# Kernel tuning notes

Hardware: AMD Instinct MI355X
Metric: run time of the kernel (lower is better)

The kernel has to match this reference:

```python
import jax, jax.numpy as jnp
import numpy as np

B, N, D, L = 64, 2047, 512, 4
T = D + 1        # token_dim = d + 1
H = 512          # hidden_dim
LN_EPS = 1e-5
ATTN_EPS = 1e-6


def setup_inputs() -> dict:
    key = jax.random.key(0)
    ks = jax.random.split(key, 10)
    s = 0.01  # matches xavier_uniform_ gain=0.01 small-init magnitude
    return dict(
        xs=jax.random.normal(ks[0], (B, N, D), jnp.float32),
        ys=jax.random.normal(ks[1], (B, N), jnp.float32),
        query_x=jax.random.normal(ks[2], (B, 1, D), jnp.float32),
        Wq=jax.random.normal(ks[3], (L, H, T), jnp.float32) * s,
        Wk=jax.random.normal(ks[4], (L, H, T), jnp.float32) * s,
        Wv=jax.random.normal(ks[5], (L, T, T), jnp.float32) * s,
        Wo=jax.random.normal(ks[6], (L, T, T), jnp.float32) * s,
        ln1_w=jnp.ones((L, T), jnp.float32),
        ln1_b=jnp.zeros((L, T), jnp.float32),
        ln2_w=jnp.ones((L, T), jnp.float32),
        ln2_b=jnp.zeros((L, T), jnp.float32),
        scale=jnp.ones((L,), jnp.float32),
        pred_w=jax.random.normal(ks[7], (1, T), jnp.float32) * 0.02,
    )


def _ln(x, w, b):
    m = jnp.mean(x, axis=-1, keepdims=True)
    v = jnp.var(x, axis=-1, keepdims=True)
    return (x - m) * jax.lax.rsqrt(v + LN_EPS) * w + b


def _l2norm(x):
    n = jnp.sqrt(jnp.sum(x * x, axis=-1, keepdims=True))
    return x / jnp.maximum(n, 1e-12)


def _forward(xs, ys, query_x, Wq, Wk, Wv, Wo, ln1_w, ln1_b, ln2_w, ln2_b, scale, pred_w):
    b = xs.shape[0]
    train_tokens = jnp.concatenate([xs, ys[..., None]], axis=-1)          # [B,N,T]
    query_token = jnp.concatenate([query_x, jnp.zeros((b, 1, 1), xs.dtype)], axis=-1)
    tokens = jnp.concatenate([train_tokens, query_token], axis=1)          # [B,N+1,T]

    def step(tok, p):
        wq, wk, wv, wo, w1, b1, w2, b2, sc = p
        x = _ln(tok, w1, b1)
        Q = jnp.einsum('bnt,ht->bnh', x, wq)
        K = jnp.einsum('bnt,ht->bnh', x, wk)
        V = jnp.einsum('bnt,ut->bnu', x, wv)
        Q = _l2norm(Q)
        K = _l2norm(K)
        s = jax.nn.softplus(sc)
        Qp = (jax.nn.elu(Q) + 1.0) * s
        Kp = jax.nn.elu(K) + 1.0
        KV = jnp.einsum('bnh,bnu->bhu', Kp, V)      # [B,H,T]
        Ksum = jnp.sum(Kp, axis=1)                  # [B,H]
        denom = jnp.einsum('bnh,bh->bn', Qp, Ksum)  # [B,N+1]
        attn = jnp.einsum('bnh,bhu->bnu', Qp, KV) / (denom[..., None] + ATTN_EPS)
        out = jnp.einsum('bnu,tu->bnt', attn, wo) * 0.1 + tok
        return _ln(out, w2, b2), None

    tokens, _ = jax.lax.scan(step, tokens, (Wq, Wk, Wv, Wo, ln1_w, ln1_b, ln2_w, ln2_b, scale))
    q_out = tokens[:, -1, :]                        # [B,T]
    return jnp.einsum('bt,ot->bo', q_out, pred_w)[..., 0]  # [B]


def reference(xs, ys, query_x, Wq, Wk, Wv, Wo, ln1_w, ln1_b, ln2_w, ln2_b, scale, pred_w):
    return _forward(xs, ys, query_x, Wq, Wk, Wv, Wo, ln1_w, ln1_b, ln2_w, ln2_b, scale, pred_w)
```

## Files before the change

kernel.cpp:

```cpp
#include <hip/hip_runtime.h>
#include <cstdint>
#include <cstddef>


typedef unsigned short u16;
typedef float f32x4 __attribute__((ext_vector_type(4)));
typedef unsigned short u16x8 __attribute__((ext_vector_type(8)));

#define P 576
#define NQK 1664
#define VTROWS 514
#define KVLD 640

__device__ __forceinline__ float bf2f(u16 s) {
    union { unsigned u; float f; } v; v.u = ((unsigned)s) << 16; return v.f;
}
__device__ __forceinline__ u16 f2bf(float f) {
    union { float f; unsigned u; } v; v.f = f;
    unsigned r = v.u + 0x7FFF + ((v.u >> 16) & 1);
    return (u16)(r >> 16);
}
__device__ __forceinline__ float wredsum(float v) {
#pragma unroll
    for (int o = 32; o > 0; o >>= 1) v += __shfl_xor(v, o, 64);
    return v;
}
__device__ __forceinline__ f32x4 mfma_16x16x32_bf16(u16x8 a, u16x8 b, f32x4 c) {
    asm volatile("v_mfma_f32_16x16x32_bf16 %0, %1, %2, %0"
                 : "+v"(c) : "v"(a), "v"(b));
    return c;
}
__device__ __forceinline__ void gload_lds16(const u16* g, u16* l) {
    __builtin_amdgcn_global_load_lds(
        (const __attribute__((address_space(1))) void*)g,
        (__attribute__((address_space(3))) void*)l, 16, 0, 0);
}

__global__ __launch_bounds__(256) void k_build_tokens(
    const float* __restrict__ xs, const float* __restrict__ ys,
    const float* __restrict__ qx, u16* __restrict__ tok,
    float* __restrict__ meanb, float* __restrict__ rstdb)
{
    long row = (long)blockIdx.x * 4 + (threadIdx.x >> 6);
    int lane = threadIdx.x & 63;
    int b = (int)(row >> 11), n = (int)(row & 2047);
    const float* src = (n < 2047) ? xs + ((long)(b * 2047 + n)) * 512
                                  : qx + (long)b * 512;
    float4 f0 = *(const float4*)(src + lane * 8);
    float4 f1 = *(const float4*)(src + lane * 8 + 4);
    float y = (n < 2047) ? ys[(long)b * 2047 + n] : 0.f;
    float v[8] = {f0.x, f0.y, f0.z, f0.w, f1.x, f1.y, f1.z, f1.w};
    float s = 0.f, sq = 0.f;
#pragma unroll
    for (int j = 0; j < 8; j++) { s += v[j]; sq += v[j] * v[j]; }
    if (lane == 0) { s += y; sq += y * y; }
    s = wredsum(s); sq = wredsum(sq);
    u16x8 o;
#pragma unroll
    for (int j = 0; j < 8; j++) o[j] = f2bf(v[j]);
    *(u16x8*)(tok + row * P + lane * 8) = o;
    if (lane < 8) {
        u16x8 z8 = {0,0,0,0,0,0,0,0};
        if (lane == 0) z8[0] = f2bf(y);
        *(u16x8*)(tok + row * P + 512 + lane * 8) = z8;
    }
    if (lane == 0) {
        float m = s * (1.f / 513.f);
        float var = sq * (1.f / 513.f) - m * m;
        meanb[row] = m;
        rstdb[row] = 1.f / sqrtf(var + 1e-5f);
    }
}

__global__ __launch_bounds__(256) void k_prep_wcat(
    const float* __restrict__ wq, const float* __restrict__ wk,
    const float* __restrict__ wv, const float* __restrict__ ln1w,
    u16* __restrict__ wcat)
{
    long idx = (long)blockIdx.x * 256 + threadIdx.x;
    if (idx >= 4L * NQK * P) return;
    int t = (int)(idx % P);
    long rem = idx / P;
    int r = (int)(rem % NQK);
    int l = (int)(rem / NQK);
    float v = 0.f;
    if (t < 513) {
        float wsc = ln1w[l * 513 + t];
        if (r < 512)       v = wq[((long)l * 512 + r) * 513 + t] * wsc;
        else if (r < 1024) v = wk[((long)l * 512 + (r - 512)) * 513 + t] * wsc;
        else if (r < 1537) v = wv[((long)l * 513 + (r - 1024)) * 513 + t] * wsc;
    }
    wcat[idx] = f2bf(v);
}

__global__ __launch_bounds__(256) void k_prep_wo(
    const float* __restrict__ wo, u16* __restrict__ wop)
{
    long idx = (long)blockIdx.x * 256 + threadIdx.x;
    if (idx >= 4L * P * P) return;
    int u = (int)(idx % P);
    long rem = idx / P;
    int t = (int)(rem % P);
    int l = (int)(rem / P);
    float v = (t < 513 && u < 513) ? wo[((long)l * 513 + t) * 513 + u] : 0.f;
    wop[idx] = f2bf(v);
}

__global__ __launch_bounds__(256) void k_prep_sums(
    const float* __restrict__ wq, const float* __restrict__ wk,
    const float* __restrict__ wv, const float* __restrict__ ln1w,
    const float* __restrict__ ln1b, float* __restrict__ s1, float* __restrict__ s2)
{
    int id = blockIdx.x * 4 + (threadIdx.x >> 6);
    int lane = threadIdx.x & 63;
    int l = id / NQK, r = id % NQK;
    float a1 = 0.f, a2 = 0.f;
    for (int t = lane; t < 513; t += 64) {
        float wc = 0.f;
        if (r < 512)       wc = wq[((long)l * 512 + r) * 513 + t];
        else if (r < 1024) wc = wk[((long)l * 512 + (r - 512)) * 513 + t];
        else if (r < 1537) wc = wv[((long)l * 513 + (r - 1024)) * 513 + t];
        a1 += ln1w[l * 513 + t] * wc;
        a2 += ln1b[l * 513 + t] * wc;
    }
    a1 = wredsum(a1); a2 = wredsum(a2);
    if (lane == 0) { s1[id] = a1; s2[id] = a2; }
}

__global__ __launch_bounds__(256) void k_ln2(
    const u16* __restrict__ z, u16* __restrict__ tok,
    const float* __restrict__ w, const float* __restrict__ bia,
    float* __restrict__ meanb, float* __restrict__ rstdb)
{
    long row = (long)blockIdx.x * 4 + (threadIdx.x >> 6);
    int lane = threadIdx.x & 63;
    const u16* zp = z + row * P;
    u16* tp = tok + row * P;
    u16x8 a0 = *(const u16x8*)(zp + lane * 8);
    u16x8 a1 = {0,0,0,0,0,0,0,0};
    if (lane < 8) a1 = *(const u16x8*)(zp + 512 + lane * 8);
    float v0[8], v1[8];
#pragma unroll
    for (int j = 0; j < 8; j++) v0[j] = bf2f(a0[j]);
#pragma unroll
    for (int j = 0; j < 8; j++) v1[j] = (lane < 8) ? bf2f(a1[j]) : 0.f;
    float s = 0.f, sq = 0.f;
#pragma unroll
    for (int j = 0; j < 8; j++) { s += v0[j]; sq += v0[j] * v0[j]; }
#pragma unroll
    for (int j = 0; j < 8; j++) { s += v1[j]; sq += v1[j] * v1[j]; }
    s = wredsum(s); sq = wredsum(sq);
    float mean = s * (1.f / 513.f);
    float var = sq * (1.f / 513.f) - mean * mean;
    float rstd = 1.f / sqrtf(var + 1e-5f);
    float so = 0.f, so2 = 0.f;
    u16x8 o0;
    float of0[8];
#pragma unroll
    for (int j = 0; j < 8; j++) {
        int t = lane * 8 + j;
        of0[j] = (v0[j] - mean) * rstd * w[t] + bia[t];
        so += of0[j]; so2 += of0[j] * of0[j];
        o0[j] = f2bf(of0[j]);
    }
    float of1[8];
#pragma unroll
    for (int j = 0; j < 8; j++) {
        int t = 512 + lane * 8 + j;
        float ov = 0.f;
        if (lane < 8 && t < 513) ov = (v1[j] - mean) * rstd * w[t] + bia[t];
        of1[j] = ov;
        so += ov; so2 += ov * ov;
    }
    so = wredsum(so); so2 = wredsum(so2);
    *(u16x8*)(tp + lane * 8) = o0;
    if (lane < 8) {
        u16x8 o1;
#pragma unroll
        for (int j = 0; j < 8; j++) o1[j] = f2bf(of1[j]);
        *(u16x8*)(tp + 512 + lane * 8) = o1;
    }
    if (lane == 0) {
        float m2 = so * (1.f / 513.f);
        float v2 = so2 * (1.f / 513.f) - m2 * m2;
        meanb[row] = m2;
        rstdb[row] = 1.f / sqrtf(v2 + 1e-5f);
    }
}

__global__ __launch_bounds__(256) void k_qknorm(
    u16* __restrict__ qkv, float* __restrict__ rkout,
    const float* __restrict__ scale, int l)
{
    long row = (long)blockIdx.x * 4 + (threadIdx.x >> 6);
    int lane = threadIdx.x & 63;
    float s = log1pf(expf(scale[l]));
    u16* rowp = qkv + row * NQK;
    u16x8 q8 = *(const u16x8*)(rowp + lane * 8);
    u16x8 k8 = *(const u16x8*)(rowp + 512 + lane * 8);
    float qf[8];
    float sqv = 0.f, skv = 0.f;
#pragma unroll
    for (int j = 0; j < 8; j++) { qf[j] = bf2f(q8[j]); sqv += qf[j] * qf[j]; }
#pragma unroll
    for (int j = 0; j < 8; j++) { float kf = bf2f(k8[j]); skv += kf * kf; }
    sqv = wredsum(sqv); skv = wredsum(skv);
    float rnq = 1.f / fmaxf(sqrtf(sqv), 1e-12f);
    float rnk = 1.f / fmaxf(sqrtf(skv), 1e-12f);
    u16x8 o;
#pragma unroll
    for (int j = 0; j < 8; j++) {
        float q = qf[j] * rnq;
        float qp = (q > 0.f) ? (q + 1.f) : expf(q);
        o[j] = f2bf(qp * s);
    }
    *(u16x8*)(rowp + lane * 8) = o;
    if (lane == 0) rkout[row] = rnk;
}

__global__ __launch_bounds__(256) void k_trans(
    const u16* __restrict__ qkv, const float* __restrict__ rk,
    u16* __restrict__ kpt)
{
    int ct = blockIdx.x;
    long r0 = (long)blockIdx.y * 64;
    int b = (int)(r0 >> 11);
    int nloc = (int)(r0 & 2047);
    int tid = threadIdx.x;
    int r = tid >> 2;
    int c0 = (tid & 3) * 16;
    __shared__ u16 T[64 * 80];
    const u16* src = qkv + (r0 + r) * NQK + 512 + ct * 64 + c0;
    u16x8 a = *(const u16x8*)src;
    u16x8 d = *(const u16x8*)(src + 8);
    float rkv = rk[r0 + r];
#pragma unroll
    for (int j = 0; j < 8; j++) {
        float kv = bf2f(a[j]) * rkv; kv = (kv > 0.f) ? kv + 1.f : expf(kv);
        T[(c0 + j) * 80 + r] = f2bf(kv);
    }
#pragma unroll
    for (int j = 0; j < 8; j++) {
        float kv = bf2f(d[j]) * rkv; kv = (kv > 0.f) ? kv + 1.f : expf(kv);
        T[(c0 + 8 + j) * 80 + r] = f2bf(kv);
    }
    __syncthreads();
    int orow = tid >> 2;
    int oc0 = (tid & 3) * 16;
    u16x8 w0 = *(const u16x8*)&T[orow * 80 + oc0];
    u16x8 w1 = *(const u16x8*)&T[orow * 80 + oc0 + 8];
    u16* dst = kpt + ((long)b * 512 + ct * 64 + orow) * 2048 + nloc + oc0;
    *(u16x8*)dst = w0;
    *(u16x8*)(dst + 8) = w1;
}

__global__ __launch_bounds__(512) void k_extract_ksum(
    const u16* __restrict__ kvh, float* __restrict__ ksum)
{
    int b = blockIdx.x, h = threadIdx.x;
    ksum[(long)b * 512 + h] = bf2f(kvh[((long)b * 512 + h) * KVLD + 513]);
}

__global__ __launch_bounds__(256) void k_denom(
    const u16* __restrict__ qkv, const float* __restrict__ ksum,
    float* __restrict__ denom)
{
    long row = (long)blockIdx.x * 4 + (threadIdx.x >> 6);
    int lane = threadIdx.x & 63;
    int b = (int)(row >> 11);
    u16x8 q = *(const u16x8*)(qkv + row * NQK + lane * 8);
    const float* ks = ksum + (long)b * 512 + lane * 8;
    float acc = 0.f;
#pragma unroll
    for (int j = 0; j < 8; j++) acc += bf2f(q[j]) * ks[j];
    acc = wredsum(acc);
    if (lane == 0) denom[row] = acc;
}

__global__ void k_predict(const u16* __restrict__ tok, const float* __restrict__ pw,
                          float* __restrict__ out)
{
    int b = blockIdx.x;
    int lane = threadIdx.x;
    const u16* rp = tok + ((long)b * 2048 + 2047) * P;
    float acc = 0.f;
    for (int t = lane; t < 513; t += 64) acc += bf2f(rp[t]) * pw[t];
    acc = wredsum(acc);
    if (lane == 0) out[b] = acc;
}

__global__ __launch_bounds__(256) void k_gemm_bt(
    const u16* __restrict__ A, const u16* __restrict__ Bt, u16* __restrict__ C,
    int M, int N, int K, int lda, int ldb, int ldc,
    long sA, long sB, long sC,
    const float* __restrict__ aux1, const float* __restrict__ aux2,
    const float* __restrict__ aux3, const float* __restrict__ aux4,
    long sAux, const u16* __restrict__ Res,
    float cscale, int mode, int r1, int padw,
    int ntm, int ntn, int nbz,
    u16* __restrict__ VT, int vtbase)
{
    int G = ntm * ntn * nbz;
    int id = blockIdx.x;
    int lin = (id & 7) * (G >> 3) + (id >> 3);
    int per = ntm * ntn;
    int bz = lin / per;
    int rem = lin - bz * per;
    int mt = rem / ntn;
    int nt = rem - mt * ntn;
    int m0 = mt * 128, n0 = nt * 128;

    A += (long)bz * sA; Bt += (long)bz * sB; C += (long)bz * sC;
    int tid = threadIdx.x, lane = tid & 63, w = tid >> 6;
    int wr = w >> 1, wc = w & 1;
    __shared__ u16 ldsbuf[2 * 128 * 64];
    u16* Als = ldsbuf;
    u16* Bls = ldsbuf + 128 * 64;
    __shared__ float auxR0[128], auxR1[128], auxA1[128];
    __shared__ float auxC0[128], auxC1[128], auxB1[128];

    if (tid < 128) {
        int gr = m0 + tid; if (gr >= M) gr = M - 1;
        float r0v = cscale, r1v = 0.f, a1v = 0.f;
        if (mode == 1) {
            const float* d1 = aux1 + (long)bz * sAux;
            r0v = cscale / (d1[gr] + 1e-6f);
        } else if (mode == 3) { r0v = aux1[gr]; r1v = aux2[gr]; }
        if (r1) a1v = bf2f(A[(long)gr * lda + K]);
        auxR0[tid] = r0v; auxR1[tid] = r1v; auxA1[tid] = a1v;
    } else {
        int t = tid - 128;
        int gc = n0 + t; if (gc >= N) gc = N - 1;
        float c0v = 0.f, c1v = 0.f, b1v = 0.f;
        if (mode == 3) { c0v = aux3[gc]; c1v = aux4[gc]; }
        if (r1) b1v = bf2f(Bt[(long)gc * ldb + K]);
        auxC0[t] = c0v; auxC1[t] = c1v; auxB1[t] = b1v;
    }

    f32x4 acc[4][4];
#pragma unroll
    for (int m = 0; m < 4; m++)
#pragma unroll
        for (int n = 0; n < 4; n++) { acc[m][n][0]=0.f; acc[m][n][1]=0.f; acc[m][n][2]=0.f; acc[m][n][3]=0.f; }

    int srow = lane >> 3;
    int scol = (lane & 7) * 8;
    int scolsw = scol ^ (srow << 3);
    int swz = (lane & 7) << 3;

    for (int k0 = 0; k0 < K; k0 += 64) {
#pragma unroll
        for (int i = 0; i < 4; i++) {
            int rt = (w * 4 + i) * 8 + srow;
            int gr = m0 + rt; gr = (gr < M) ? gr : (M - 1);
            gload_lds16(A + (long)gr * lda + k0 + scolsw, &Als[(w * 4 + i) * 512]);
        }
#pragma unroll
        for (int i = 0; i < 4; i++) {
            int rt = (w * 4 + i) * 8 + srow;
            int gc = n0 + rt; gc = (gc < N) ? gc : (N - 1);
            gload_lds16(Bt + (long)gc * ldb + k0 + scolsw, &Bls[(w * 4 + i) * 512]);
        }
        __syncthreads();
#pragma unroll
        for (int ks = 0; ks < 2; ks++) {
            u16x8 af[4], bfv[4];
#pragma unroll
            for (int m = 0; m < 4; m++) {
                int row = wr * 64 + m * 16 + (lane & 15);
                af[m] = *(const u16x8*)&Als[row * 64 + ((ks * 32 + (lane >> 4) * 8) ^ swz)];
            }
#pragma unroll
            for (int n = 0; n < 4; n++) {
                int col = wc * 64 + n * 16 + (lane & 15);
                bfv[n] = *(const u16x8*)&Bls[col * 64 + ((ks * 32 + (lane >> 4) * 8) ^ swz)];
            }
#pragma unroll
            for (int m = 0; m < 4; m++)
#pragma unroll
                for (int n = 0; n < 4; n++)
                    acc[m][n] = mfma_16x16x32_bf16(af[m], bfv[n], acc[m][n]);
        }
        __syncthreads();
    }

    bool isvt = (VT != nullptr) && (n0 >= vtbase);

    if (Res) {
        const u16* Rp = Res + (long)bz * sC;
#pragma unroll
        for (int i = 0; i < 8; i++) {
            int lrow = i * 16 + (tid >> 4);
            int lcol = (tid & 15) * 8;
            long gr = m0 + lrow; if (gr > (long)M - 1) gr = M - 1;
            long gcol = (long)n0 + lcol;
            long mx = (long)ldc - 8; if (gcol > mx) gcol = mx;
            *(u16x8*)&ldsbuf[lrow * 128 + lcol] = *(const u16x8*)&Rp[gr * ldc + gcol];
        }
        __syncthreads();
    }

    asm volatile("s_nop 7\n\ts_nop 7" ::: );

    if (!isvt) {
#pragma unroll
        for (int m = 0; m < 4; m++) {
            int lrbase = wr * 64 + m * 16 + ((lane >> 4) << 2);
#pragma unroll
            for (int n = 0; n < 4; n++) {
                int lc = wc * 64 + n * 16 + (lane & 15);
                float c0v = auxC0[lc], c1v = auxC1[lc], b1v = auxB1[lc];
#pragma unroll
                for (int r = 0; r < 4; r++) {
                    int lr = lrbase + r;
                    float wv = acc[m][n][r] + auxA1[lr] * b1v;
                    float v;
                    if (mode == 3) v = auxR1[lr] * (wv - auxR0[lr] * c0v) + c1v;
                    else {
                        v = wv * auxR0[lr];
                        if (Res) v += bf2f(ldsbuf[lr * 128 + lc]);
                    }
                    ldsbuf[lr * 128 + lc] = f2bf(v);
                }
            }
        }
        __syncthreads();

        int lcol = (tid & 15) * 8;
        int gc0 = n0 + lcol;
        bool colok = padw || (gc0 + 8 <= N);
#pragma unroll
        for (int i = 0; i < 8; i++) {
            int lrow = i * 16 + (tid >> 4);
            int gr = m0 + lrow;
            if (gr < M && colok) {
                *(u16x8*)&C[(long)gr * ldc + gc0] = *(const u16x8*)&ldsbuf[lrow * 128 + lcol];
            }
        }
    } else {
        int u0 = n0 - vtbase;
        int b = m0 >> 11;
        int nloc = m0 & 2047;
#pragma unroll
        for (int m = 0; m < 4; m++) {
            int lrbase = wr * 64 + m * 16 + ((lane >> 4) << 2);
#pragma unroll
            for (int n = 0; n < 4; n++) {
                int lc = wc * 64 + n * 16 + (lane & 15);
                float c0v = auxC0[lc], c1v = auxC1[lc];
#pragma unroll
                for (int r = 0; r < 4; r++) {
                    int lr = lrbase + r;
                    float wv = acc[m][n][r];
                    float v = (mode == 3) ? (auxR1[lr] * (wv - auxR0[lr] * c0v) + c1v)
                                          : (wv * auxR0[lr]);
                    ldsbuf[lc * 128 + (lr ^ ((lc & 7) << 3))] = f2bf(v);
                }
            }
        }
        __syncthreads();

        int nc = (tid & 15) * 8;
        const u16x8 ones = {0x3F80,0x3F80,0x3F80,0x3F80,0x3F80,0x3F80,0x3F80,0x3F80};
#pragma unroll
        for (int i = 0; i < 8; i++) {
            int ur = i * 16 + (tid >> 4);
            int u = u0 + ur;
            if (u < VTROWS) {
                u16x8 vv;
                if (u == 513) vv = ones;
                else vv = *(const u16x8*)&ldsbuf[ur * 128 + (nc ^ ((ur & 7) << 3))];
                *(u16x8*)&VT[((long)b * VTROWS + u) * 2048 + nloc + nc] = vv;
            }
        }
    }
}

extern "C" void kernel_launch(void* const* d_in, const int* in_sizes, int n_in,
                              void* d_out, int out_size, void* d_ws, size_t ws_size,
                              hipStream_t stream)
{
    const float* xs    = (const float*)d_in[0];
    const float* ys    = (const float*)d_in[1];
    const float* qx    = (const float*)d_in[2];
    const float* Wq    = (const float*)d_in[3];
    const float* Wk    = (const float*)d_in[4];
    const float* Wv    = (const float*)d_in[5];
    const float* Wo    = (const float*)d_in[6];
    const float* ln1w  = (const float*)d_in[7];
    const float* ln1b  = (const float*)d_in[8];
    const float* ln2w  = (const float*)d_in[9];
    const float* ln2b  = (const float*)d_in[10];
    const float* scale = (const float*)d_in[11];
    const float* predw = (const float*)d_in[12];
    float* out = (float*)d_out;

    char* ws = (char*)d_ws;
    u16*   tok   = (u16*)(ws + 0L);
    u16*   buf1  = (u16*)(ws + 150994944L);
    u16*   qkv   = (u16*)(ws + 301989888L);
    u16*   kpt   = (u16*)(ws + 738197504L);
    u16*   kvh   = (u16*)(ws + 872415232L);
    float* denom = (float*)(ws + 914358272L);
    float* meanb = (float*)(ws + 914882560L);
    float* rstdb = (float*)(ws + 915406848L);
    float* ksum  = (float*)(ws + 915931136L);
    u16*   wcat  = (u16*)(ws + 916062208L);
    u16*   wop   = (u16*)(ws + 923729920L);
    float* s1    = (float*)(ws + 926384128L);
    float* s2    = (float*)(ws + 926410752L);
    float* rkb   = (float*)(ws + 301465600L);
    u16*   w2t   = kpt;

    k_build_tokens<<<32768, 256, 0, stream>>>(xs, ys, qx, tok, meanb, rstdb);
    {
        long n1 = 4L * NQK * P;
        k_prep_wcat<<<(int)((n1 + 255) / 256), 256, 0, stream>>>(Wq, Wk, Wv, ln1w, wcat);
        long n2 = 4L * P * P;
        k_prep_wo<<<(int)((n2 + 255) / 256), 256, 0, stream>>>(Wo, wop);
        k_prep_sums<<<1664, 256, 0, stream>>>(Wq, Wk, Wv, ln1w, ln1b, s1, s2);
    }

    for (int l = 0; l < 4; l++) {
        k_gemm_bt<<<13312, 256, 0, stream>>>(tok, wcat + (long)l * NQK * P, qkv,
            131072, NQK, 576, P, P, NQK, 0, 0, 0,
            meanb, rstdb, s1 + l * NQK, s2 + l * NQK, 0, nullptr,
            1.f, 3, 0, 0, 1024, 13, 1,
            buf1, 1024);
        k_qknorm<<<32768, 256, 0, stream>>>(qkv, rkb, scale, l);
        {
            dim3 g(8, 2048, 1);
            k_trans<<<g, 256, 0, stream>>>(qkv, rkb, kpt);
        }
        k_gemm_bt<<<1280, 256, 0, stream>>>(kpt, buf1, kvh,
            512, VTROWS, 2048, 2048, 2048, KVLD,
            512L * 2048, (long)VTROWS * 2048, 512L * KVLD,
            nullptr, nullptr, nullptr, nullptr, 0, nullptr, 1.f, 0, 0, 1,
            4, 5, 64, nullptr, 1 << 30);
        k_extract_ksum<<<64, 512, 0, stream>>>(kvh, ksum);
        k_denom<<<32768, 256, 0, stream>>>(qkv, ksum, denom);
        k_gemm_bt<<<1280, 256, 0, stream>>>(wop + (long)l * P * P, kvh, w2t,
            576, 512, 512, P, KVLD, 512,
            0, 512L * KVLD, 576L * 512,
            nullptr, nullptr, nullptr, nullptr, 0, nullptr, 1.f, 0, 1, 0,
            5, 4, 64, nullptr, 1 << 30);
        k_gemm_bt<<<5120, 256, 0, stream>>>(qkv, w2t, buf1,
            2048, P, 512, NQK, 512, P,
            2048L * NQK, 576L * 512, 2048L * P,
            denom, nullptr, nullptr, nullptr, 2048, tok,
            0.1f, 1, 0, 0, 16, 5, 64, nullptr, 1 << 30);
        k_ln2<<<32768, 256, 0, stream>>>(buf1, tok, ln2w + l * 513, ln2b + l * 513,
                                         meanb, rstdb);
    }
    k_predict<<<64, 64, 0, stream>>>(tok, predw, out);
}
```

Before: 3.496 ms.

## Add dedicated 256x256-tile pipelined QKV GEMM kernel with fused LN epilogue

Replaces the generic batched GEMM for the per-layer QKV projection with a specialized 512-thread kernel. It uses 256x256 output tiles, double-buffered LDS staging via direct global-to-LDS loads, swizzled LDS layout, and a four-phase interleaving of loads with MFMA. The LayerNorm-folded epilogue writes Q/K rows through LDS, and writes the V block transposed into the VT buffer along with a ones row. The aim is to raise arithmetic intensity and overlap memory with compute for the largest GEMM. The trade-off is heavy register and LDS use (about 132KB dynamic shared memory) and clamped out-of-range columns in the last N tile.

```diff
diff --git a/kernel.cpp b/kernel.cpp
--- a/kernel.cpp
+++ b/kernel.cpp
@@ -287,6 +287,190 @@
     for (int t = lane; t < 513; t += 64) acc += bf2f(rp[t]) * pw[t];
     acc = wredsum(acc);
     if (lane == 0) out[b] = acc;
+}
+
+#define QN 1664
+
+#define QSTAGE(DB, HALF, K0)                                                   \
+    {                                                                          \
+        _Pragma("unroll")                                                      \
+        for (int j = 0; j < 2; j++) {                                          \
+            int row_ = j * 64 + srow;                                          \
+            const u16* src_;                                                   \
+            if ((HALF) < 2) {                                                  \
+                src_ = Ag + (long)(m0 + (HALF) * 128 + row_) * 576 + (K0) + colsw; \
+            } else {                                                           \
+                int gc_ = n0 + ((HALF) - 2) * 128 + row_;                      \
+                if (gc_ >= QN) gc_ = QN - 1;                                   \
+                src_ = Bg + (long)gc_ * 576 + (K0) + colsw;                    \
+            }                                                                  \
+            gload_lds16(src_, S + (DB) * 32768 + (HALF) * 8192 + j * 4096 + w * 512); \
+        }                                                                      \
+    }
+
+#define QLDA(AH)                                                               \
+    _Pragma("unroll")                                                          \
+    for (int m_ = 0; m_ < 4; m_++) {                                           \
+        int rr_ = wr * 64 + m_ * 16 + (lane & 15);                             \
+        _Pragma("unroll")                                                      \
+        for (int ks_ = 0; ks_ < 2; ks_++)                                      \
+            af[m_][ks_] = *(const u16x8*)&Bc[(AH) * 8192 + rr_ * 64 +          \
+                          ((ks_ * 32 + (lane >> 4) * 8) ^ swz)];               \
+    }
+
+#define QLDB(BH)                                                               \
+    _Pragma("unroll")                                                          \
+    for (int n_ = 0; n_ < 2; n_++) {                                           \
+        int cc_ = wc * 32 + n_ * 16 + (lane & 15);                             \
+        _Pragma("unroll")                                                      \
+        for (int ks_ = 0; ks_ < 2; ks_++)                                      \
+            bf[n_][ks_] = *(const u16x8*)&Bc[16384 + (BH) * 8192 + cc_ * 64 +  \
+                          ((ks_ * 32 + (lane >> 4) * 8) ^ swz)];               \
+    }
+
+#define QPHASE(AH, BH, RDA, RDB, SHALF)                                        \
+    __builtin_amdgcn_sched_barrier(0);                                         \
+    if (RDA) { QLDA(AH) }                                                      \
+    if (RDB) { QLDB(BH) }                                                      \
+    QSTAGE(nb, SHALF, k1)                                                      \
+    asm volatile("s_waitcnt vmcnt(4)" ::: "memory");                           \
+    __builtin_amdgcn_s_barrier();                                              \
+    __builtin_amdgcn_s_setprio(1);                                             \
+    _Pragma("unroll")                                                          \
+    for (int m_ = 0; m_ < 4; m_++)                                             \
+        _Pragma("unroll")                                                      \
+        for (int n_ = 0; n_ < 2; n_++) {                                       \
+            acc[AH][BH][m_][n_] =                                              \
+                mfma_16x16x32_bf16(af[m_][0], bf[n_][0], acc[AH][BH][m_][n_]); \
+            acc[AH][BH][m_][n_] =                                              \
+                mfma_16x16x32_bf16(af[m_][1], bf[n_][1], acc[AH][BH][m_][n_]); \
+        }                                                                      \
+    __builtin_amdgcn_s_setprio(0);                                             \
+    __builtin_amdgcn_s_barrier();
+
+__global__ __launch_bounds__(512, 2) void k_qkv8(
+    const u16* __restrict__ Ag, const u16* __restrict__ Bg, u16* __restrict__ C,
+    const float* __restrict__ meanb, const float* __restrict__ rstdb,
+    const float* __restrict__ s1l, const float* __restrict__ s2l,
+    u16* __restrict__ VT)
+{
+    extern __shared__ u16 S[];
+    int id = blockIdx.x;
+    int lin = (id & 7) * 448 + (id >> 3);
+    int mt = lin / 7, nt = lin - mt * 7;
+    int m0 = mt * 256, n0 = nt * 256;
+    int tid = threadIdx.x, lane = tid & 63, w = tid >> 6;
+    int wr = w >> 2, wc = w & 3;
+
+    float* auxp = (float*)(S + 65536);
+    if (tid < 256) {
+        auxp[tid] = meanb[(long)m0 + tid];
+        auxp[256 + tid] = rstdb[(long)m0 + tid];
+    } else {
+        int t = tid - 256;
+        int gc = n0 + t; if (gc >= QN) gc = QN - 1;
+        auxp[512 + t] = s1l[gc];
+        auxp[768 + t] = s2l[gc];
+    }
+
+    int srow = (w << 3) + (lane >> 3);
+    int colsw = ((lane & 7) << 3) ^ ((lane >> 3) << 3);
+    int swz = (lane & 7) << 3;
+
+    f32x4 acc[2][2][4][2];
+#pragma unroll
+    for (int a_ = 0; a_ < 2; a_++)
+#pragma unroll
+    for (int b_ = 0; b_ < 2; b_++)
+#pragma unroll
+    for (int m_ = 0; m_ < 4; m_++)
+#pragma unroll
+    for (int n_ = 0; n_ < 2; n_++) {
+        acc[a_][b_][m_][n_][0] = 0.f; acc[a_][b_][m_][n_][1] = 0.f;
+        acc[a_][b_][m_][n_][2] = 0.f; acc[a_][b_][m_][n_][3] = 0.f;
+    }
+    u16x8 af[4][2], bf[2][2];
+
+    QSTAGE(0, 0, 0) QSTAGE(0, 2, 0) QSTAGE(0, 3, 0) QSTAGE(0, 1, 0)
+    asm volatile("s_waitcnt vmcnt(4)" ::: "memory");
+    __builtin_amdgcn_s_barrier();
+
+    for (int kt = 0; kt < 9; ++kt) {
+        u16* Bc = S + (kt & 1) * 32768;
+        int nb = (kt & 1) ^ 1;
+        int k1 = (kt >= 8 ? 8 : kt + 1) * 64;
+        QPHASE(0, 0, 1, 1, 0)
+        QPHASE(0, 1, 0, 1, 2)
+        QPHASE(1, 1, 1, 0, 3)
+        QPHASE(1, 0, 0, 1, 1)
+    }
+    asm volatile("s_waitcnt vmcnt(0)" ::: "memory");
+    __builtin_amdgcn_s_barrier();
+
+    if (n0 < 1024) {
+#pragma unroll
+        for (int ah = 0; ah < 2; ah++)
+#pragma unroll
+        for (int bh = 0; bh < 2; bh++)
+#pragma unroll
+        for (int m_ = 0; m_ < 4; m_++)
+#pragma unroll
+        for (int n_ = 0; n_ < 2; n_++) {
+            int lr0 = ah * 128 + wr * 64 + m_ * 16 + ((lane >> 4) << 2);
+            int lc = bh * 128 + wc * 32 + n_ * 16 + (lane & 15);
+            float s1c = auxp[512 + lc], s2c = auxp[768 + lc];
+#pragma unroll
+            for (int r_ = 0; r_ < 4; r_++) {
+                int lr = lr0 + r_;
+                float v = auxp[256 + lr] * (acc[ah][bh][m_][n_][r_]
+                          - auxp[lr] * s1c) + s2c;
+                S[lr * 256 + (lc ^ ((lr & 7) << 3))] = f2bf(v);
+            }
+        }
+        __syncthreads();
+#pragma unroll
+        for (int i = 0; i < 16; i++) {
+            int g = i * 512 + tid;
+            int row = g >> 5, c0 = (g & 31) * 8;
+            *(u16x8*)&C[(long)(m0 + row) * 1664 + n0 + c0] =
+                *(const u16x8*)&S[row * 256 + (c0 ^ ((row & 7) << 3))];
+        }
+    } else {
+        int u0 = n0 - 1024, b = m0 >> 11, nloc = m0 & 2047;
+#pragma unroll
+        for (int ah = 0; ah < 2; ah++)
+#pragma unroll
+        for (int bh = 0; bh < 2; bh++)
+#pragma unroll
+        for (int m_ = 0; m_ < 4; m_++)
+#pragma unroll
+        for (int n_ = 0; n_ < 2; n_++) {
+            int lr0 = ah * 128 + wr * 64 + m_ * 16 + ((lane >> 4) << 2);
+            int lc = bh * 128 + wc * 32 + n_ * 16 + (lane & 15);
+            float s1c = auxp[512 + lc], s2c = auxp[768 + lc];
+#pragma unroll
+            for (int r_ = 0; r_ < 4; r_++) {
+                int lr = lr0 + r_;
+                float v = auxp[256 + lr] * (acc[ah][bh][m_][n_][r_]
+                          - auxp[lr] * s1c) + s2c;
+                S[lc * 256 + (lr ^ ((lc & 7) << 3))] = f2bf(v);
+            }
+        }
+        __syncthreads();
+        const u16x8 ones = {0x3F80,0x3F80,0x3F80,0x3F80,0x3F80,0x3F80,0x3F80,0x3F80};
+#pragma unroll
+        for (int i = 0; i < 16; i++) {
+            int g = i * 512 + tid;
+            int ur = g >> 5, t0 = (g & 31) * 8;
+            int u = u0 + ur;
+            if (u < VTROWS) {
+                u16x8 vv;
+                if (u == 513) vv = ones;
+                else vv = *(const u16x8*)&S[ur * 256 + (t0 ^ ((ur & 7) << 3))];
+                *(u16x8*)&VT[((long)b * VTROWS + u) * 2048 + nloc + t0] = vv;
+            }
+        }
+    }
 }
 
 __global__ __launch_bounds__(256) void k_gemm_bt(
@@ -512,6 +696,13 @@
     float* rkb   = (float*)(ws + 301465600L);
     u16*   w2t   = kpt;
 
+    static bool attr_done = false;
+    if (!attr_done) {
+        (void)hipFuncSetAttribute((const void*)k_qkv8,
+            hipFuncAttributeMaxDynamicSharedMemorySize, 135168);
+        attr_done = true;
+    }
+
     k_build_tokens<<<32768, 256, 0, stream>>>(xs, ys, qx, tok, meanb, rstdb);
     {
         long n1 = 4L * NQK * P;
@@ -522,11 +713,8 @@
     }
 
     for (int l = 0; l < 4; l++) {
-        k_gemm_bt<<<13312, 256, 0, stream>>>(tok, wcat + (long)l * NQK * P, qkv,
-            131072, NQK, 576, P, P, NQK, 0, 0, 0,
-            meanb, rstdb, s1 + l * NQK, s2 + l * NQK, 0, nullptr,
-            1.f, 3, 0, 0, 1024, 13, 1,
-            buf1, 1024);
+        k_qkv8<<<3584, 512, 135168, stream>>>(tok, wcat + (long)l * NQK * P, qkv,
+            meanb, rstdb, s1 + l * NQK, s2 + l * NQK, buf1);
         k_qknorm<<<32768, 256, 0, stream>>>(qkv, rkb, scale, l);
         {
             dim3 g(8, 2048, 1);
```

Result: no change. 3.494 ms (-0.0%).
